# Kernel tuning notes

Measured on AMD Instinct MI355X. Metric: run time of the kernel, lower is better.

## Reference

```python
import jax, jax.numpy as jnp
import numpy as np

B, S, D, E, K = 4, 2048, 1024, 8, 2
LN_EPS = 1e-5


def setup_inputs() -> dict:
    key = jax.random.key(0)
    ks = jax.random.split(key, 8)
    s = 1.0 / np.sqrt(D)
    return {
        "x": jax.random.normal(ks[0], (B, S, D), dtype=jnp.float32),
        "noise": jax.random.normal(ks[1], (B, S, E), dtype=jnp.float32) * (1.0 / E),
        "W_route": jax.random.uniform(ks[2], (D, E), minval=-s, maxval=s, dtype=jnp.float32),
        "b_route": jax.random.uniform(ks[3], (E,), minval=-s, maxval=s, dtype=jnp.float32),
        "ln_gamma": jnp.ones((E,), dtype=jnp.float32),
        "ln_beta": jnp.zeros((E,), dtype=jnp.float32),
        "W_exp": jax.random.uniform(ks[4], (E, D, D), minval=-s, maxval=s, dtype=jnp.float32),
        "b_exp": jax.random.uniform(ks[5], (E, D), minval=-s, maxval=s, dtype=jnp.float32),
    }


def reference(x, noise, W_route, b_route, ln_gamma, ln_beta, W_exp, b_exp):
    # Routing: Linear(dim, E) -> LayerNorm(E) -> softmax, plus noise
    logits = jnp.einsum("bsd,de->bse", x, W_route) + b_route
    mu = logits.mean(axis=-1, keepdims=True)
    var = logits.var(axis=-1, keepdims=True)
    ln = (logits - mu) / jnp.sqrt(var + LN_EPS) * ln_gamma + ln_beta
    routing = jax.nn.softmax(ln, axis=-1) + noise

    topk_w, topk_i = jax.lax.top_k(routing, K)          # [B,S,K]
    topk_w = jax.nn.softmax(topk_w, axis=-1)

    # Dense all-expert compute (faithful to the naive original)
    expert_out = jnp.einsum("bsd,edf->bsef", x, W_exp) + b_exp  # [B,S,E,D]

    # Gather top-k experts per token and combine
    sel = jnp.take_along_axis(expert_out, topk_i[..., None], axis=2)  # [B,S,K,D]
    return (sel * topk_w[..., None]).sum(axis=2)
```

## Files before the change

kernel.cpp:

```cpp
#include <hip/hip_runtime.h>
#include <hip/hip_bf16.h>


typedef unsigned short u16;
typedef __bf16 bf16x8 __attribute__((ext_vector_type(8)));
typedef float floatx4 __attribute__((ext_vector_type(4)));
typedef unsigned short u16x8 __attribute__((ext_vector_type(8)));

#define NTOK 8192
#define DDIM 1024
#define NEXP 8

__device__ __forceinline__ u16 f2bf(float f) {
    union { float f; unsigned int i; } c; c.f = f;
    unsigned int i = c.i;
    return (u16)((i + 0x7fffu + ((i >> 16) & 1u)) >> 16);
}

__global__ __launch_bounds__(256) void transpose_w(const float* __restrict__ W,
                                                   u16* __restrict__ WT) {
    __shared__ __align__(16) u16 tile[64][72];
    const int e = blockIdx.z, d0 = blockIdx.y * 64, f0 = blockIdx.x * 64;
    const int t = threadIdx.x;
    const float* src = W + (size_t)e * DDIM * DDIM;
    u16* dst = WT + (size_t)e * DDIM * DDIM;
#pragma unroll
    for (int it = 0; it < 2; ++it) {
        int idx = it * 256 + t;
        int r = idx >> 3, c8 = idx & 7;
        const float* sp = src + (size_t)(d0 + r) * DDIM + f0 + c8 * 8;
        float4 va = *(const float4*)sp;
        float4 vb = *(const float4*)(sp + 4);
        u16x8 v;
        v[0] = f2bf(va.x); v[1] = f2bf(va.y); v[2] = f2bf(va.z); v[3] = f2bf(va.w);
        v[4] = f2bf(vb.x); v[5] = f2bf(vb.y); v[6] = f2bf(vb.z); v[7] = f2bf(vb.w);
        *(u16x8*)&tile[r][c8 * 8] = v;
    }
    __syncthreads();
#pragma unroll
    for (int it = 0; it < 2; ++it) {
        int idx = it * 256 + t;
        int fr = idx >> 3, d8 = idx & 7;
        u16x8 o;
#pragma unroll
        for (int j = 0; j < 8; ++j) o[j] = tile[d8 * 8 + j][fr];
        *(u16x8*)(dst + (size_t)(f0 + fr) * DDIM + d0 + d8 * 8) = o;
    }
}

__global__ __launch_bounds__(256) void routing_compute(
    const float* __restrict__ x, const float* __restrict__ noise,
    const float* __restrict__ Wr, const float* __restrict__ br,
    const float* __restrict__ gamma, const float* __restrict__ beta,
    int* __restrict__ e01, float2* __restrict__ w01) {
    __shared__ __align__(16) float wrT[NEXP][DDIM];
    const int t = threadIdx.x;
#pragma unroll
    for (int i = 0; i < 8; ++i) {
        int f4 = i * 256 + t;
        int d = f4 >> 1, half = (f4 & 1) * 4;
        float4 v = *(const float4*)&Wr[d * 8 + half];
        wrT[half + 0][d] = v.x; wrT[half + 1][d] = v.y;
        wrT[half + 2][d] = v.z; wrT[half + 3][d] = v.w;
    }
    __syncthreads();

    const int wave = t >> 6, lane = t & 63;
    const int tok = blockIdx.x * 4 + wave;
    const float4* xrow = (const float4*)(x + (size_t)tok * DDIM);
    float acc[8];
#pragma unroll
    for (int e = 0; e < 8; ++e) acc[e] = 0.f;
#pragma unroll
    for (int i = 0; i < 4; ++i) {
        int d4 = i * 64 + lane;
        float4 xv = xrow[d4];
#pragma unroll
        for (int e = 0; e < 8; ++e) {
            float4 wv = *(const float4*)&wrT[e][d4 * 4];
            acc[e] += xv.x * wv.x + xv.y * wv.y + xv.z * wv.z + xv.w * wv.w;
        }
    }
#pragma unroll
    for (int off = 32; off >= 1; off >>= 1) {
#pragma unroll
        for (int e = 0; e < 8; ++e) acc[e] += __shfl_xor(acc[e], off, 64);
    }
    if (lane == 0) {
        float lg[8], mu = 0.f;
#pragma unroll
        for (int e = 0; e < 8; ++e) { lg[e] = acc[e] + br[e]; mu += lg[e]; }
        mu *= 0.125f;
        float var = 0.f;
#pragma unroll
        for (int e = 0; e < 8; ++e) { float d = lg[e] - mu; var += d * d; }
        var *= 0.125f;
        float rstd = rsqrtf(var + 1e-5f);
        float ln[8], mx = -1e30f;
#pragma unroll
        for (int e = 0; e < 8; ++e) {
            ln[e] = (lg[e] - mu) * rstd * gamma[e] + beta[e];
            mx = fmaxf(mx, ln[e]);
        }
        float s = 0.f, p[8];
#pragma unroll
        for (int e = 0; e < 8; ++e) { p[e] = expf(ln[e] - mx); s += p[e]; }
        float inv = 1.f / s, r[8];
#pragma unroll
        for (int e = 0; e < 8; ++e) r[e] = p[e] * inv + noise[(size_t)tok * 8 + e];
        int i0 = 0; float v0 = r[0];
#pragma unroll
        for (int e = 1; e < 8; ++e) if (r[e] > v0) { v0 = r[e]; i0 = e; }
        int i1 = -1; float v1 = -1e30f;
#pragma unroll
        for (int e = 0; e < 8; ++e) if (e != i0 && r[e] > v1) { v1 = r[e]; i1 = e; }
        float w0 = 1.f / (1.f + expf(v1 - v0));
        e01[tok] = i0 | (i1 << 8);
        w01[tok] = make_float2(w0, 1.f - w0);
    }
}

__global__ __launch_bounds__(256) void build_lists(
    const int* __restrict__ e01, const float2* __restrict__ w01,
    int* __restrict__ counts, int* __restrict__ list_tok, float* __restrict__ list_w) {
    const int g = blockIdx.x;
    const int slot = g >> 3, ex = g & 7;
    const int t = threadIdx.x, wave = t >> 6, lane = t & 63;
    __shared__ int wtot[4];
    int base = 0;
    for (int start = 0; start < NTOK; start += 256) {
        int tok = start + t;
        int packed = e01[tok];
        int e = slot ? ((packed >> 8) & 0xff) : (packed & 0xff);
        bool sel = (e == ex);
        unsigned long long m = __ballot(sel);
        int prefix = __popcll(m & ((1ULL << lane) - 1ULL));
        if (lane == 0) wtot[wave] = __popcll(m);
        __syncthreads();
        int wbase = 0;
#pragma unroll
        for (int wv = 0; wv < 4; ++wv) if (wv < wave) wbase += wtot[wv];
        int total = wtot[0] + wtot[1] + wtot[2] + wtot[3];
        if (sel) {
            float2 w2 = w01[tok];
            int pos = base + wbase + prefix;
            list_tok[g * NTOK + pos] = tok;
            list_w[g * NTOK + pos] = slot ? w2.y : w2.x;
        }
        base += total;
        __syncthreads();
    }
    if (t == 0) counts[g] = base;
}

__global__ __launch_bounds__(256) void moe_gemm(
    const float* __restrict__ x, const u16* __restrict__ WT,
    const float* __restrict__ bexp, const int* __restrict__ counts,
    const int* __restrict__ list_tok, const float* __restrict__ list_w,
    float* __restrict__ out, int grp_base, int accum) {
    const int e = blockIdx.z;
    const int grp = grp_base + e;
    int cnt = counts[grp];
    cnt = cnt < 0 ? 0 : (cnt > NTOK ? NTOK : cnt);
    const int m0 = blockIdx.y * 128;
    if (m0 >= cnt) return;
    const int n0 = blockIdx.x * 128;

    __shared__ __align__(16) u16 A_s[128 * 32];
    __shared__ __align__(16) u16 B_s[128 * 32];
    __shared__ int tok_s[128];
    __shared__ float w_s[128];
    __shared__ float bias_s[128];

    const int t = threadIdx.x;
    if (t < 128) {
        int r = m0 + t;
        int rr = r < cnt ? r : cnt - 1;
        tok_s[t] = list_tok[grp * NTOK + rr] & (NTOK - 1);
        w_s[t] = (r < cnt) ? list_w[grp * NTOK + rr] : 0.f;
        bias_s[t] = bexp[e * DDIM + n0 + t];
    }
    __syncthreads();

    const int ra = t >> 2;
    const int co = (t & 3) * 8;
    const float* xg0 = x + (size_t)tok_s[ra] * DDIM + co;
    const float* xg1 = x + (size_t)tok_s[64 + ra] * DDIM + co;
    const u16* wg0 = WT + ((size_t)e * DDIM + n0 + ra) * DDIM + co;
    const u16* wg1 = WT + ((size_t)e * DDIM + n0 + 64 + ra) * DDIM + co;
    u16* sA0 = A_s + ra * 32 + co;
    u16* sA1 = A_s + (64 + ra) * 32 + co;
    u16* sB0 = B_s + ra * 32 + co;
    u16* sB1 = B_s + (64 + ra) * 32 + co;

    const int lane = t & 63, wave = t >> 6;
    const int wm = wave >> 1, wn = wave & 1;
    const int lm = lane & 15;
    const int ko = (lane >> 4) * 8;

    floatx4 acc[4][4];
#pragma unroll
    for (int mi = 0; mi < 4; ++mi)
#pragma unroll
        for (int ni = 0; ni < 4; ++ni) acc[mi][ni] = (floatx4){0.f, 0.f, 0.f, 0.f};

    for (int kk = 0; kk < DDIM; kk += 32) {
        float4 fa0 = *(const float4*)(xg0 + kk);
        float4 fa0b = *(const float4*)(xg0 + kk + 4);
        float4 fa1 = *(const float4*)(xg1 + kk);
        float4 fa1b = *(const float4*)(xg1 + kk + 4);
        u16x8 b0 = *(const u16x8*)(wg0 + kk);
        u16x8 b1 = *(const u16x8*)(wg1 + kk);
        u16x8 a0, a1;
        a0[0] = f2bf(fa0.x); a0[1] = f2bf(fa0.y); a0[2] = f2bf(fa0.z); a0[3] = f2bf(fa0.w);
        a0[4] = f2bf(fa0b.x); a0[5] = f2bf(fa0b.y); a0[6] = f2bf(fa0b.z); a0[7] = f2bf(fa0b.w);
        a1[0] = f2bf(fa1.x); a1[1] = f2bf(fa1.y); a1[2] = f2bf(fa1.z); a1[3] = f2bf(fa1.w);
        a1[4] = f2bf(fa1b.x); a1[5] = f2bf(fa1b.y); a1[6] = f2bf(fa1b.z); a1[7] = f2bf(fa1b.w);
        __syncthreads();
        *(u16x8*)sA0 = a0;
        *(u16x8*)sA1 = a1;
        *(u16x8*)sB0 = b0;
        *(u16x8*)sB1 = b1;
        __syncthreads();
        bf16x8 af[4], bfr[4];
#pragma unroll
        for (int mi = 0; mi < 4; ++mi)
            af[mi] = *(const bf16x8*)&A_s[(wm * 64 + mi * 16 + lm) * 32 + ko];
#pragma unroll
        for (int ni = 0; ni < 4; ++ni)
            bfr[ni] = *(const bf16x8*)&B_s[(wn * 64 + ni * 16 + lm) * 32 + ko];
#pragma unroll
        for (int mi = 0; mi < 4; ++mi)
#pragma unroll
            for (int ni = 0; ni < 4; ++ni)
                acc[mi][ni] = __builtin_amdgcn_mfma_f32_16x16x32_bf16(
                    af[mi], bfr[ni], acc[mi][ni], 0, 0, 0);
    }

#pragma unroll
    for (int mi = 0; mi < 4; ++mi) {
        int rb = wm * 64 + mi * 16 + (lane >> 4) * 4;
#pragma unroll
        for (int reg = 0; reg < 4; ++reg) {
            int r = rb + reg;
            if (m0 + r < cnt) {
                size_t tok = (size_t)tok_s[r];
                float w = w_s[r];
                float* yrow = out + tok * DDIM + n0;
#pragma unroll
                for (int ni = 0; ni < 4; ++ni) {
                    int col = wn * 64 + ni * 16 + lm;
                    float v = w * (acc[mi][ni][reg] + bias_s[col]);
                    if (accum) v += yrow[col];
                    yrow[col] = v;
                }
            }
        }
    }
}

extern "C" void kernel_launch(void* const* d_in, const int* in_sizes, int n_in,
                              void* d_out, int out_size, void* d_ws, size_t ws_size,
                              hipStream_t stream) {
    const float* x     = (const float*)d_in[0];
    const float* noise = (const float*)d_in[1];
    const float* Wr    = (const float*)d_in[2];
    const float* br    = (const float*)d_in[3];
    const float* gamma = (const float*)d_in[4];
    const float* beta  = (const float*)d_in[5];
    const float* Wexp  = (const float*)d_in[6];
    const float* bexp  = (const float*)d_in[7];
    float* out = (float*)d_out;

    unsigned char* ws = (unsigned char*)d_ws;
    u16* WT       = (u16*)ws;
    int* counts   = (int*)(ws + 16777216);
    int* list_tok = (int*)(ws + 16777216 + 256);
    float* list_w = (float*)(ws + 16777216 + 256 + 524288);
    int* e01      = (int*)(ws + 16777216 + 256 + 1048576);
    float2* w01   = (float2*)(ws + 16777216 + 256 + 1048576 + 32768);

    transpose_w<<<dim3(16, 16, 8), 256, 0, stream>>>(Wexp, WT);
    routing_compute<<<NTOK / 4, 256, 0, stream>>>(x, noise, Wr, br, gamma, beta,
                                                  e01, w01);
    build_lists<<<16, 256, 0, stream>>>(e01, w01, counts, list_tok, list_w);
    moe_gemm<<<dim3(8, 64, 8), 256, 0, stream>>>(x, WT, bexp, counts, list_tok, list_w,
                                                 out, 0, 0);
    moe_gemm<<<dim3(8, 64, 8), 256, 0, stream>>>(x, WT, bexp, counts, list_tok, list_w,
                                                 out, 8, 1);
}
```

Baseline: 259.8 us.

## Pre-cast activations to bf16, swizzle LDS tiles, and remap GEMM block order

Adds an xcast kernel that converts x to bf16 once, so the expert GEMM loads half as many bytes per A tile and skips the per-iteration fp32-to-bf16 conversion. Shared-memory tiles get an XOR swizzle on the 16-byte chunk index to cut LDS bank conflicts on the MFMA fragment reads. The grid is flattened to 1D and remapped so consecutive blocks share M tiles across N tiles, which should improve L2 reuse of gathered token rows. The cost is an extra kernel launch and a 16 MB workspace buffer, with a fallback to the old fp32 path when the workspace is too small.

```diff
diff --git a/kernel.cpp b/kernel.cpp
--- a/kernel.cpp
+++ b/kernel.cpp
@@ -15,6 +15,21 @@
     union { float f; unsigned int i; } c; c.f = f;
     unsigned int i = c.i;
     return (u16)((i + 0x7fffu + ((i >> 16) & 1u)) >> 16);
+}
+
+__device__ __forceinline__ int swz(int row, int chunk) {
+    return row * 32 + ((chunk ^ ((row >> 1) & 3)) << 3);
+}
+
+__global__ __launch_bounds__(256) void xcast(const float* __restrict__ x,
+                                             u16* __restrict__ xb) {
+    size_t i = ((size_t)blockIdx.x * 256 + threadIdx.x) * 8;
+    float4 a = *(const float4*)(x + i);
+    float4 b = *(const float4*)(x + i + 4);
+    u16x8 v;
+    v[0] = f2bf(a.x); v[1] = f2bf(a.y); v[2] = f2bf(a.z); v[3] = f2bf(a.w);
+    v[4] = f2bf(b.x); v[5] = f2bf(b.y); v[6] = f2bf(b.z); v[7] = f2bf(b.w);
+    *(u16x8*)(xb + i) = v;
 }
 
 __global__ __launch_bounds__(256) void transpose_w(const float* __restrict__ W,
@@ -153,18 +168,23 @@
     if (t == 0) counts[g] = base;
 }
 
+template <int BF16A>
 __global__ __launch_bounds__(256) void moe_gemm(
-    const float* __restrict__ x, const u16* __restrict__ WT,
-    const float* __restrict__ bexp, const int* __restrict__ counts,
-    const int* __restrict__ list_tok, const float* __restrict__ list_w,
-    float* __restrict__ out, int grp_base, int accum) {
+    const float* __restrict__ xf, const u16* __restrict__ xb,
+    const u16* __restrict__ WT, const float* __restrict__ bexp,
+    const int* __restrict__ counts, const int* __restrict__ list_tok,
+    const float* __restrict__ list_w, float* __restrict__ out,
+    int grp_base, int accum) {
     const int e = blockIdx.z;
     const int grp = grp_base + e;
     int cnt = counts[grp];
     cnt = cnt < 0 ? 0 : (cnt > NTOK ? NTOK : cnt);
-    const int m0 = blockIdx.y * 128;
+    const int lin = blockIdx.x;
+    const int n = (lin >> 3) & 7;
+    const int m = (lin & 7) | ((lin >> 6) << 3);
+    const int m0 = m * 128;
     if (m0 >= cnt) return;
-    const int n0 = blockIdx.x * 128;
+    const int n0 = n * 128;
 
     __shared__ __align__(16) u16 A_s[128 * 32];
     __shared__ __align__(16) u16 B_s[128 * 32];
@@ -183,20 +203,19 @@
     __syncthreads();
 
     const int ra = t >> 2;
-    const int co = (t & 3) * 8;
-    const float* xg0 = x + (size_t)tok_s[ra] * DDIM + co;
-    const float* xg1 = x + (size_t)tok_s[64 + ra] * DDIM + co;
+    const int ch = t & 3;
+    const int co = ch * 8;
     const u16* wg0 = WT + ((size_t)e * DDIM + n0 + ra) * DDIM + co;
     const u16* wg1 = WT + ((size_t)e * DDIM + n0 + 64 + ra) * DDIM + co;
-    u16* sA0 = A_s + ra * 32 + co;
-    u16* sA1 = A_s + (64 + ra) * 32 + co;
-    u16* sB0 = B_s + ra * 32 + co;
-    u16* sB1 = B_s + (64 + ra) * 32 + co;
+    u16* sA0 = A_s + swz(ra, ch);
+    u16* sA1 = A_s + swz(64 + ra, ch);
+    u16* sB0 = B_s + swz(ra, ch);
+    u16* sB1 = B_s + swz(64 + ra, ch);
 
     const int lane = t & 63, wave = t >> 6;
     const int wm = wave >> 1, wn = wave & 1;
     const int lm = lane & 15;
-    const int ko = (lane >> 4) * 8;
+    const int kc = lane >> 4;
 
     floatx4 acc[4][4];
 #pragma unroll
@@ -204,18 +223,28 @@
 #pragma unroll
         for (int ni = 0; ni < 4; ++ni) acc[mi][ni] = (floatx4){0.f, 0.f, 0.f, 0.f};
 
+    const float* xg0f = xf + (size_t)tok_s[ra] * DDIM + co;
+    const float* xg1f = xf + (size_t)tok_s[64 + ra] * DDIM + co;
+    const u16* xg0b = xb + (size_t)tok_s[ra] * DDIM + co;
+    const u16* xg1b = xb + (size_t)tok_s[64 + ra] * DDIM + co;
+
     for (int kk = 0; kk < DDIM; kk += 32) {
-        float4 fa0 = *(const float4*)(xg0 + kk);
-        float4 fa0b = *(const float4*)(xg0 + kk + 4);
-        float4 fa1 = *(const float4*)(xg1 + kk);
-        float4 fa1b = *(const float4*)(xg1 + kk + 4);
+        u16x8 a0, a1;
+        if (BF16A) {
+            a0 = *(const u16x8*)(xg0b + kk);
+            a1 = *(const u16x8*)(xg1b + kk);
+        } else {
+            float4 fa0 = *(const float4*)(xg0f + kk);
+            float4 fa0b = *(const float4*)(xg0f + kk + 4);
+            float4 fa1 = *(const float4*)(xg1f + kk);
+            float4 fa1b = *(const float4*)(xg1f + kk + 4);
+            a0[0] = f2bf(fa0.x); a0[1] = f2bf(fa0.y); a0[2] = f2bf(fa0.z); a0[3] = f2bf(fa0.w);
+            a0[4] = f2bf(fa0b.x); a0[5] = f2bf(fa0b.y); a0[6] = f2bf(fa0b.z); a0[7] = f2bf(fa0b.w);
+            a1[0] = f2bf(fa1.x); a1[1] = f2bf(fa1.y); a1[2] = f2bf(fa1.z); a1[3] = f2bf(fa1.w);
+            a1[4] = f2bf(fa1b.x); a1[5] = f2bf(fa1b.y); a1[6] = f2bf(fa1b.z); a1[7] = f2bf(fa1b.w);
+        }
         u16x8 b0 = *(const u16x8*)(wg0 + kk);
         u16x8 b1 = *(const u16x8*)(wg1 + kk);
-        u16x8 a0, a1;
-        a0[0] = f2bf(fa0.x); a0[1] = f2bf(fa0.y); a0[2] = f2bf(fa0.z); a0[3] = f2bf(fa0.w);
-        a0[4] = f2bf(fa0b.x); a0[5] = f2bf(fa0b.y); a0[6] = f2bf(fa0b.z); a0[7] = f2bf(fa0b.w);
-        a1[0] = f2bf(fa1.x); a1[1] = f2bf(fa1.y); a1[2] = f2bf(fa1.z); a1[3] = f2bf(fa1.w);
-        a1[4] = f2bf(fa1b.x); a1[5] = f2bf(fa1b.y); a1[6] = f2bf(fa1b.z); a1[7] = f2bf(fa1b.w);
         __syncthreads();
         *(u16x8*)sA0 = a0;
         *(u16x8*)sA1 = a1;
@@ -225,10 +254,10 @@
         bf16x8 af[4], bfr[4];
 #pragma unroll
         for (int mi = 0; mi < 4; ++mi)
-            af[mi] = *(const bf16x8*)&A_s[(wm * 64 + mi * 16 + lm) * 32 + ko];
+            af[mi] = *(const bf16x8*)&A_s[swz(wm * 64 + mi * 16 + lm, kc)];
 #pragma unroll
         for (int ni = 0; ni < 4; ++ni)
-            bfr[ni] = *(const bf16x8*)&B_s[(wn * 64 + ni * 16 + lm) * 32 + ko];
+            bfr[ni] = *(const bf16x8*)&B_s[swz(wn * 64 + ni * 16 + lm, kc)];
 #pragma unroll
         for (int mi = 0; mi < 4; ++mi)
 #pragma unroll
@@ -275,17 +304,28 @@
     unsigned char* ws = (unsigned char*)d_ws;
     u16* WT       = (u16*)ws;
     int* counts   = (int*)(ws + 16777216);
-    int* list_tok = (int*)(ws + 16777216 + 256);
-    float* list_w = (float*)(ws + 16777216 + 256 + 524288);
-    int* e01      = (int*)(ws + 16777216 + 256 + 1048576);
-    float2* w01   = (float2*)(ws + 16777216 + 256 + 1048576 + 32768);
+    int* list_tok = (int*)(ws + 16777472);
+    float* list_w = (float*)(ws + 17301760);
+    int* e01      = (int*)(ws + 17826048);
+    float2* w01   = (float2*)(ws + 17858816);
+    u16* xb       = (u16*)(ws + 17924352);
+    const size_t need_bf16a = 17924352 + 16777216;
 
     transpose_w<<<dim3(16, 16, 8), 256, 0, stream>>>(Wexp, WT);
     routing_compute<<<NTOK / 4, 256, 0, stream>>>(x, noise, Wr, br, gamma, beta,
                                                   e01, w01);
     build_lists<<<16, 256, 0, stream>>>(e01, w01, counts, list_tok, list_w);
-    moe_gemm<<<dim3(8, 64, 8), 256, 0, stream>>>(x, WT, bexp, counts, list_tok, list_w,
-                                                 out, 0, 0);
-    moe_gemm<<<dim3(8, 64, 8), 256, 0, stream>>>(x, WT, bexp, counts, list_tok, list_w,
-                                                 out, 8, 1);
-}
+
+    if (ws_size >= need_bf16a) {
+        xcast<<<NTOK * DDIM / (256 * 8), 256, 0, stream>>>(x, xb);
+        moe_gemm<1><<<dim3(512, 1, 8), 256, 0, stream>>>(
+            x, xb, WT, bexp, counts, list_tok, list_w, out, 0, 0);
+        moe_gemm<1><<<dim3(512, 1, 8), 256, 0, stream>>>(
+            x, xb, WT, bexp, counts, list_tok, list_w, out, 8, 1);
+    } else {
+        moe_gemm<0><<<dim3(512, 1, 8), 256, 0, stream>>>(
+            x, xb, WT, bexp, counts, list_tok, list_w, out, 0, 0);
+        moe_gemm<0><<<dim3(512, 1, 8), 256, 0, stream>>>(
+            x, xb, WT, bexp, counts, list_tok, list_w, out, 8, 1);
+    }
+}
```

New measurement: 253.4 us. 1.03x faster.
